# Optimization experiments

Hardware: AMD Instinct MI355X
Metric: run time of the kernel (lower is better)

Reference implementation:

```python
import jax, jax.numpy as jnp
import numpy as np

SIZE_DICT = 512
DIM_DICT = 64
TEMPERATURE = 0.5
EPS = 1e-10


def setup_inputs() -> dict:
    key = jax.random.key(0)
    k1, k2, k3 = jax.random.split(key, 3)
    bs, dz, W, H = 32, 64, 32, 32
    z = jax.random.normal(k1, (bs, dz, W, H), dtype=jnp.float32)
    var_q = jnp.ones((1,), dtype=jnp.float32)
    codebook = jax.random.normal(k2, (SIZE_DICT, DIM_DICT), dtype=jnp.float32)
    gumbel_u = jax.random.uniform(k3, (bs * W * H, SIZE_DICT), dtype=jnp.float32)
    return {"z_from_encoder": z, "var_q": var_q, "codebook": codebook, "gumbel_u": gumbel_u}


def reference(z_from_encoder, var_q, codebook, gumbel_u):
    bs, dz, W, H = z_from_encoder.shape
    # permute to channels-last and flatten: [N, D]
    z_flat = jnp.transpose(z_from_encoder, (0, 2, 3, 1)).reshape(-1, dz)
    # precision with clamping as in torch code
    precision_q = jnp.clip(1.0 / jnp.clip(var_q, 1e-5, None), None, 1e5)  # [1]
    half_prec = 0.5 * precision_q
    # squared euclidean distances to codebook: [N, K]
    dist = (jnp.sum(z_flat ** 2, axis=1, keepdims=True)
            + jnp.sum(codebook ** 2, axis=1)
            - 2.0 * z_flat @ codebook.T)
    logit = -half_prec * dist
    logit = logit - jnp.max(logit, axis=-1, keepdims=True)
    logit = jnp.clip(logit, -50.0, 50.0)
    probabilities = jax.nn.softmax(logit, axis=-1)
    log_probabilities = jax.nn.log_softmax(logit, axis=-1)
    # Gumbel-softmax sampling (training path)
    g = -jnp.log(-jnp.log(gumbel_u + EPS) + EPS)
    encodings = jax.nn.softmax((logit + g) / TEMPERATURE, axis=-1)
    # soft codebook lookup
    z_quantized = (encodings @ codebook).reshape(bs, W, H, dz)
    z_to_decoder = jnp.transpose(z_quantized, (0, 3, 1, 2))  # [bs, D, W, H]
    # discrete KLD term: sum_{n,k} p log p / bs
    kld_discrete = jnp.sum(probabilities * log_probabilities) / bs
    # continuous KLD term: mean over batch of weighted squared error
    kld_continuous = jnp.mean(
        jnp.sum((z_from_encoder - z_to_decoder) ** 2 * half_prec, axis=(1, 2, 3)))
    loss = kld_discrete + kld_continuous
    # perplexity from detached probabilities
    avg_probs = jnp.clip(jnp.mean(jax.lax.stop_gradient(probabilities), axis=0), 1e-10, None)
    perplexity = jnp.exp(-jnp.sum(avg_probs * jnp.log(avg_probs + 1e-10)))
    return z_to_decoder, loss, perplexity
```

## Files before the change

kernel.cpp:

```cpp
#include <hip/hip_runtime.h>


typedef _Float16 half8 __attribute__((ext_vector_type(8)));
typedef float f32x4 __attribute__((ext_vector_type(4)));

#define WS_B1   4096
#define WS_B2   20480
#define WS_PROB 36864
#define WS_LOSS 299008
#define WS_RED  303104
#define WS_NEED 319488

#define ZC_OFF  0
#define ES_OFF  9216
#define ZQ_OFF  50176
#define PR_OFF  83968
#define RM_OFF  86016
#define RS_OFF  87040
#define RP_OFF  88064
#define LB_OFF  89088
#define SMEM_PRE 89152
#define SMEM_FB  155136

#define LOG2E 1.4426950408889634f
#define LN2   0.6931471805599453f
#define C2G   1.4426950408889634e-10f

__device__ __forceinline__ float half_prec(const float* var_q) {
  float vq = var_q[0];
  float pq = fminf(1.0f / fmaxf(vq, 1e-5f), 1e5f);
  return 0.5f * pq;
}

__global__ void k_pre(const float* __restrict__ var_q,
                      const float* __restrict__ cb,
                      float* __restrict__ ws, int pre) {
  int t = threadIdx.x, wg = blockIdx.x;
  if (wg == 0) {
    float hp = half_prec(var_q);
    if (t == 0) ws[512] = 0.0f;
    ws[516 + t] = 0.0f;
    const float4* row = (const float4*)(cb + t * 64);
    float s = 0.0f;
    #pragma unroll
    for (int i = 0; i < 16; ++i) {
      float4 v = row[i];
      s += v.x*v.x + v.y*v.y + v.z*v.z + v.w*v.w;
    }
    ws[t] = hp * s * LOG2E;
  }
  if (!pre) return;
  int gid = wg * 512 + t;
  if (gid < 4096) {
    int l = gid & 63, grp = gid >> 6;
    int tt = grp >> 1, kk = grp & 1;
    int cc = l & 15, gg = l >> 4;
    const float* src = cb + (cc*32 + tt)*64 + kk*32 + gg*8;
    float4 v0 = *(const float4*)src;
    float4 v1 = *(const float4*)(src + 4);
    half8 h = { (_Float16)v0.x, (_Float16)v0.y, (_Float16)v0.z, (_Float16)v0.w,
                (_Float16)v1.x, (_Float16)v1.y, (_Float16)v1.z, (_Float16)v1.w };
    ((half8*)(ws + WS_B1))[gid] = h;
  } else {
    int F = gid - 4096;
    int l = F & 63, grp = F >> 6;
    int kt = grp >> 2, nt = grp & 3;
    int cc = l & 15, gg = l >> 4;
    int dim = nt*16 + cc;
    half8 h;
    #pragma unroll
    for (int j = 0; j < 8; ++j) {
      int kap = gg*8 + j;
      int code = ((kap & 15) << 5) + 2*kt + (kap >> 4);
      h[j] = (_Float16)cb[code*64 + dim];
    }
    ((half8*)(ws + WS_B2))[F] = h;
  }
}

__global__ __launch_bounds__(1024) void k_main_pre(
    const float* __restrict__ z, const float* __restrict__ vq,
    const float* __restrict__ cb, const float* __restrict__ gu,
    float* __restrict__ out, float* __restrict__ ws)
{
  extern __shared__ char smem[];
  float* pr   = (float*)(smem + PR_OFF);
  float* redM = (float*)(smem + RM_OFF);
  float* redS = (float*)(smem + RS_OFF);
  float* redP = (float*)(smem + RP_OFF);
  float* lb   = (float*)(smem + LB_OFF);

  const int tid  = threadIdx.x;
  const int lane = tid & 63;
  const int wv   = tid >> 6;
  const int e    = wv & 3;
  const int p    = wv >> 2;
  const int c    = lane & 15;
  const int g    = lane >> 4;

  if (tid < 512) pr[tid] = 0.0f;

  const half8* B1 = (const half8*)(ws + WS_B1);
  const half8* B2 = (const half8*)(ws + WS_B2);

  const float hp   = half_prec(vq);
  const float s2hp = 2.0f * hp * LOG2E;

  const int row0 = (blockIdx.x * 4 + p) * 16;
  const int b    = row0 >> 10;
  const int wh0  = row0 & 1023;

  _Float16* zc = (_Float16*)(smem + ZC_OFF + p * 2304);

  float zr[4];
  {
    const float* zp = z + ((size_t)(b*64 + lane) << 10) + wh0 + 4*e;
    float4 v0 = *(const float4*)zp;
    zr[0]=v0.x; zr[1]=v0.y; zr[2]=v0.z; zr[3]=v0.w;
  }
  #pragma unroll
  for (int s = 0; s < 4; ++s) zc[(4*e + s)*72 + lane] = (_Float16)(zr[s] * s2hp);

  __syncthreads();

  f32x4 acc[8];
  {
    const float4* hn = (const float4*)(ws + c*32 + 8*e);
    #pragma unroll
    for (int u = 0; u < 2; ++u) {
      float4 h4 = hn[u];
      acc[4*u+0] = (f32x4){-h4.x, -h4.x, -h4.x, -h4.x};
      acc[4*u+1] = (f32x4){-h4.y, -h4.y, -h4.y, -h4.y};
      acc[4*u+2] = (f32x4){-h4.z, -h4.z, -h4.z, -h4.z};
      acc[4*u+3] = (f32x4){-h4.w, -h4.w, -h4.w, -h4.w};
    }
  }

  half8 zA0 = *(const half8*)(zc + c*72 + g*8);
  half8 zA1 = *(const half8*)(zc + c*72 + 32 + g*8);

  #pragma unroll
  for (int t = 0; t < 8; ++t) {
    int tt = 8*e + t;
    acc[t] = __builtin_amdgcn_mfma_f32_16x16x32_f16(zA0, B1[(tt*2+0)*64 + lane], acc[t], 0, 0, 0);
    acc[t] = __builtin_amdgcn_mfma_f32_16x16x32_f16(zA1, B1[(tt*2+1)*64 + lane], acc[t], 0, 0, 0);
  }

  const int rix = p*64 + e*16;

  #pragma unroll
  for (int q = 0; q < 4; ++q) {
    float m = acc[0][q];
    #pragma unroll
    for (int t = 1; t < 8; ++t) m = fmaxf(m, acc[t][q]);
    #pragma unroll
    for (int o = 8; o > 0; o >>= 1) m = fmaxf(m, __shfl_xor(m, o));
    if (c == 0) redM[rix + 4*g + q] = m;
  }
  __syncthreads();
  float mq[4];
  #pragma unroll
  for (int q = 0; q < 4; ++q) {
    int ix = p*64 + 4*g + q;
    mq[q] = fmaxf(fmaxf(redM[ix], redM[ix+16]), fmaxf(redM[ix+32], redM[ix+48]));
  }

  {
    float s1[4] = {0,0,0,0}, pl[4] = {0,0,0,0};
    #pragma unroll
    for (int t = 0; t < 8; ++t)
      #pragma unroll
      for (int q = 0; q < 4; ++q) {
        float l = acc[t][q] - mq[q];
        float ev = exp2f(l);
        s1[q] += ev;
        pl[q] = fmaf(ev, l, pl[q]);
        acc[t][q] = ev;
      }
    #pragma unroll
    for (int q = 0; q < 4; ++q) {
      #pragma unroll
      for (int o = 8; o > 0; o >>= 1) { s1[q] += __shfl_xor(s1[q], o); pl[q] += __shfl_xor(pl[q], o); }
      if (c == 0) { redS[rix + 4*g + q] = s1[q]; redP[rix + 4*g + q] = pl[q]; }
    }
  }
  __syncthreads();
  float kd = 0.0f, inv1[4];
  #pragma unroll
  for (int q = 0; q < 4; ++q) {
    int ix = p*64 + 4*g + q;
    float S = (redS[ix] + redS[ix+16]) + (redS[ix+32] + redS[ix+48]);
    float P = (redP[ix] + redP[ix+16]) + (redP[ix+32] + redP[ix+48]);
    inv1[q] = 1.0f / S;
    kd += P * inv1[q] - __log2f(S);
  }

  #pragma unroll
  for (int t = 0; t < 8; ++t) {
    float v = 0.0f;
    #pragma unroll
    for (int q = 0; q < 4; ++q) v = fmaf(acc[t][q], inv1[q], v);
    v += __shfl_xor(v, 16);
    v += __shfl_xor(v, 32);
    if (g == 0) atomicAdd(&pr[(8*e + t)*16 + c], v);
  }

  #pragma unroll
  for (int q = 0; q < 4; ++q) {
    const float4* ub = (const float4*)(gu + ((size_t)(row0 + 4*g + q))*512 + c*32 + 8*e);
    #pragma unroll
    for (int tt = 0; tt < 2; ++tt) {
      float4 u4 = ub[tt];
      float y0 = C2G - __log2f(u4.x + 1e-10f);
      float y1 = C2G - __log2f(u4.y + 1e-10f);
      float y2 = C2G - __log2f(u4.z + 1e-10f);
      float y3 = C2G - __log2f(u4.w + 1e-10f);
      float t0 = acc[4*tt+0][q] * __builtin_amdgcn_rcpf(y0);
      float t1 = acc[4*tt+1][q] * __builtin_amdgcn_rcpf(y1);
      float t2 = acc[4*tt+2][q] * __builtin_amdgcn_rcpf(y2);
      float t3 = acc[4*tt+3][q] * __builtin_amdgcn_rcpf(y3);
      acc[4*tt+0][q] = t0*t0;
      acc[4*tt+1][q] = t1*t1;
      acc[4*tt+2][q] = t2*t2;
      acc[4*tt+3][q] = t3*t3;
    }
  }

  __syncthreads();

  #pragma unroll
  for (int q = 0; q < 4; ++q) {
    float s = 0.0f;
    #pragma unroll
    for (int t = 0; t < 8; ++t) s += acc[t][q];
    #pragma unroll
    for (int o = 8; o > 0; o >>= 1) s += __shfl_xor(s, o);
    if (c == 0) redS[rix + 4*g + q] = s;
  }
  __syncthreads();
  #pragma unroll
  for (int q = 0; q < 4; ++q) {
    int ix = p*64 + 4*g + q;
    float inv = 1.0f / ((redS[ix] + redS[ix+16]) + (redS[ix+32] + redS[ix+48]));
    #pragma unroll
    for (int t = 0; t < 8; ++t) acc[t][q] *= inv;
  }

  f32x4 zacc[4];
  #pragma unroll
  for (int nt = 0; nt < 4; ++nt) zacc[nt] = (f32x4){0.f, 0.f, 0.f, 0.f};

  _Float16* myES = (_Float16*)(smem + ES_OFF + wv * 2560);
  #pragma unroll
  for (int k = 0; k < 4; ++k) {
    _Float16* eS = myES + (k & 1) * 640;
    #pragma unroll
    for (int tb = 0; tb < 2; ++tb)
      #pragma unroll
      for (int q = 0; q < 4; ++q)
        eS[(4*g + q)*40 + 16*tb + c] = (_Float16)acc[2*k + tb][q];
    half8 ea = *(const half8*)(eS + c*40 + g*8);
    int kt = 4*e + k;
    #pragma unroll
    for (int nt = 0; nt < 4; ++nt)
      zacc[nt] = __builtin_amdgcn_mfma_f32_16x16x32_f16(ea, B2[(kt*4 + nt)*64 + lane], zacc[nt], 0, 0, 0);
  }

  float* zqA = (float*)(smem + ZQ_OFF + p * 8448);
  float* zqB = zqA + 1056;
  if (e & 1) {
    float* zqX = (e == 1) ? zqA : zqB;
    #pragma unroll
    for (int nt = 0; nt < 4; ++nt)
      #pragma unroll
      for (int q = 0; q < 4; ++q)
        zqX[(4*g + q)*66 + nt*16 + c] = zacc[nt][q];
  }
  __syncthreads();
  if (!(e & 1)) {
    float* zqX = (e == 0) ? zqA : zqB;
    #pragma unroll
    for (int nt = 0; nt < 4; ++nt)
      #pragma unroll
      for (int q = 0; q < 4; ++q)
        zqX[(4*g + q)*66 + nt*16 + c] += zacc[nt][q];
  }
  __syncthreads();

  float kc = 0.0f;
  {
    float* orow = out + ((size_t)(b*64 + lane) << 10) + wh0 + 4*e;
    float4 ov;
    ov.x = zqA[(4*e + 0)*66 + lane] + zqB[(4*e + 0)*66 + lane];
    ov.y = zqA[(4*e + 1)*66 + lane] + zqB[(4*e + 1)*66 + lane];
    ov.z = zqA[(4*e + 2)*66 + lane] + zqB[(4*e + 2)*66 + lane];
    ov.w = zqA[(4*e + 3)*66 + lane] + zqB[(4*e + 3)*66 + lane];
    float d;
    d = zr[0]-ov.x; kc = fmaf(d,d,kc);  d = zr[1]-ov.y; kc = fmaf(d,d,kc);
    d = zr[2]-ov.z; kc = fmaf(d,d,kc);  d = zr[3]-ov.w; kc = fmaf(d,d,kc);
    *(float4*)orow = ov;
  }
  kc *= hp;

  float lv = ((e == 0) ? kd * (0.0625f * LN2) : 0.0f) + kc;
  #pragma unroll
  for (int o = 32; o > 0; o >>= 1) lv += __shfl_xor(lv, o);
  if (lane == 0) lb[p*4 + e] = lv;
  __syncthreads();
  if (e == 0 && lane == 0)
    ws[WS_LOSS + blockIdx.x*4 + p] = (lb[p*4+0] + lb[p*4+1]) + (lb[p*4+2] + lb[p*4+3]);

  if (tid < 512) ws[WS_PROB + (size_t)blockIdx.x*512 + tid] = pr[tid];
}

__global__ __launch_bounds__(512) void k_main_fb(
    const float* __restrict__ z, const float* __restrict__ vq,
    const float* __restrict__ cb, const float* __restrict__ gu,
    float* __restrict__ out, float* __restrict__ ws)
{
  extern __shared__ char smem[];
  constexpr int CB = 131072;
  char*  chunkAll = smem + CB;
  float* pr   = (float*)(smem + CB + 20480);
  float* redM = (float*)(smem + CB + 22528);
  float* redS = (float*)(smem + CB + 23040);
  float* redP = (float*)(smem + CB + 23552);

  const int tid  = threadIdx.x;
  const int lane = tid & 63;
  const int wv   = tid >> 6;
  const int h    = wv & 1;
  const int p    = wv >> 1;
  const int c    = lane & 15;
  const int g    = lane >> 4;

  pr[tid] = 0.0f;

  _Float16* lB1 = (_Float16*)smem;
  _Float16* lB2 = (_Float16*)(smem + 65536);
  #pragma unroll
  for (int i = 0; i < 8; ++i) {
    int F = tid + 512*i;
    int l = F & 63, grp = F >> 6;
    int t = grp >> 1, kk = grp & 1;
    int cc = l & 15, gg = l >> 4;
    const float* src = cb + (cc*32 + t)*64 + kk*32 + gg*8;
    float4 v0 = *(const float4*)src;
    float4 v1 = *(const float4*)(src + 4);
    half8 hh = { (_Float16)v0.x, (_Float16)v0.y, (_Float16)v0.z, (_Float16)v0.w,
                 (_Float16)v1.x, (_Float16)v1.y, (_Float16)v1.z, (_Float16)v1.w };
    ((half8*)lB1)[F] = hh;
  }
  #pragma unroll
  for (int i = 0; i < 8; ++i) {
    int F = tid + 512*i;
    int l = F & 63, grp = F >> 6;
    int kt = grp >> 2, nt = grp & 3;
    int cc = l & 15, gg = l >> 4;
    int dim = nt*16 + cc;
    half8 hh;
    #pragma unroll
    for (int j = 0; j < 8; ++j) {
      int kap = gg*8 + j;
      int code = ((kap & 15) << 5) + 2*kt + (kap >> 4);
      hh[j] = (_Float16)cb[code*64 + dim];
    }
    ((half8*)lB2)[F] = hh;
  }
  const half8* B1 = (const half8*)lB1;
  const half8* B2 = (const half8*)lB2;

  const float hp   = half_prec(vq);
  const float s2hp = 2.0f * hp * LOG2E;

  const int row0 = (blockIdx.x * 4 + p) * 16;
  const int b    = row0 >> 10;
  const int wh0  = row0 & 1023;

  _Float16* zc = (_Float16*)(chunkAll + p * 5120);

  float zr[8];
  {
    const float* zp = z + ((size_t)(b*64 + lane) << 10) + wh0 + 8*h;
    float4 v0 = *(const float4*)zp;
    float4 v1 = *(const float4*)(zp + 4);
    zr[0]=v0.x; zr[1]=v0.y; zr[2]=v0.z; zr[3]=v0.w;
    zr[4]=v1.x; zr[5]=v1.y; zr[6]=v1.z; zr[7]=v1.w;
  }
  #pragma unroll
  for (int s = 0; s < 8; ++s) zc[(8*h + s)*72 + lane] = (_Float16)(zr[s] * s2hp);

  __syncthreads();

  f32x4 acc[16];
  {
    const float4* hn = (const float4*)(ws + c*32 + h*16);
    #pragma unroll
    for (int u = 0; u < 4; ++u) {
      float4 h4 = hn[u];
      acc[4*u+0] = (f32x4){-h4.x, -h4.x, -h4.x, -h4.x};
      acc[4*u+1] = (f32x4){-h4.y, -h4.y, -h4.y, -h4.y};
      acc[4*u+2] = (f32x4){-h4.z, -h4.z, -h4.z, -h4.z};
      acc[4*u+3] = (f32x4){-h4.w, -h4.w, -h4.w, -h4.w};
    }
  }

  half8 zA0 = *(const half8*)(zc + c*72 + g*8);
  half8 zA1 = *(const half8*)(zc + c*72 + 32 + g*8);

  #pragma unroll
  for (int t = 0; t < 16; ++t) {
    int tt = h*16 + t;
    acc[t] = __builtin_amdgcn_mfma_f32_16x16x32_f16(zA0, B1[(tt*2+0)*64 + lane], acc[t], 0, 0, 0);
    acc[t] = __builtin_amdgcn_mfma_f32_16x16x32_f16(zA1, B1[(tt*2+1)*64 + lane], acc[t], 0, 0, 0);
  }

  const int rix = p*32 + h*16;

  #pragma unroll
  for (int q = 0; q < 4; ++q) {
    float m = acc[0][q];
    #pragma unroll
    for (int t = 1; t < 16; ++t) m = fmaxf(m, acc[t][q]);
    #pragma unroll
    for (int o = 8; o > 0; o >>= 1) m = fmaxf(m, __shfl_xor(m, o));
    if (c == 0) redM[rix + 4*g + q] = m;
  }
  __syncthreads();
  float mq[4];
  #pragma unroll
  for (int q = 0; q < 4; ++q)
    mq[q] = fmaxf(redM[p*32 + 4*g + q], redM[p*32 + 16 + 4*g + q]);

  {
    float s1[4] = {0,0,0,0}, pl[4] = {0,0,0,0};
    #pragma unroll
    for (int t = 0; t < 16; ++t)
      #pragma unroll
      for (int q = 0; q < 4; ++q) {
        float l = acc[t][q] - mq[q];
        float ev = exp2f(l);
        s1[q] += ev;
        pl[q] = fmaf(ev, l, pl[q]);
        acc[t][q] = ev;
      }
    #pragma unroll
    for (int q = 0; q < 4; ++q) {
      #pragma unroll
      for (int o = 8; o > 0; o >>= 1) { s1[q] += __shfl_xor(s1[q], o); pl[q] += __shfl_xor(pl[q], o); }
      if (c == 0) { redS[rix + 4*g + q] = s1[q]; redP[rix + 4*g + q] = pl[q]; }
    }
  }
  __syncthreads();
  float kd = 0.0f, inv1[4];
  #pragma unroll
  for (int q = 0; q < 4; ++q) {
    float S = redS[p*32 + 4*g + q] + redS[p*32 + 16 + 4*g + q];
    float P = redP[p*32 + 4*g + q] + redP[p*32 + 16 + 4*g + q];
    inv1[q] = 1.0f / S;
    kd += P * inv1[q] - __log2f(S);
  }

  #pragma unroll
  for (int t = 0; t < 16; ++t) {
    float v = 0.0f;
    #pragma unroll
    for (int q = 0; q < 4; ++q) v = fmaf(acc[t][q], inv1[q], v);
    v += __shfl_xor(v, 16);
    v += __shfl_xor(v, 32);
    if (g == 0) atomicAdd(&pr[(h*16 + t)*16 + c], v);
  }

  #pragma unroll
  for (int q = 0; q < 4; ++q) {
    const float4* ub = (const float4*)(gu + ((size_t)(row0 + 4*g + q))*512 + c*32 + h*16);
    #pragma unroll
    for (int tt = 0; tt < 4; ++tt) {
      float4 u4 = ub[tt];
      float y0 = C2G - __log2f(u4.x + 1e-10f);
      float y1 = C2G - __log2f(u4.y + 1e-10f);
      float y2 = C2G - __log2f(u4.z + 1e-10f);
      float y3 = C2G - __log2f(u4.w + 1e-10f);
      float t0 = acc[4*tt+0][q] * __builtin_amdgcn_rcpf(y0);
      float t1 = acc[4*tt+1][q] * __builtin_amdgcn_rcpf(y1);
      float t2 = acc[4*tt+2][q] * __builtin_amdgcn_rcpf(y2);
      float t3 = acc[4*tt+3][q] * __builtin_amdgcn_rcpf(y3);
      acc[4*tt+0][q] = t0*t0;
      acc[4*tt+1][q] = t1*t1;
      acc[4*tt+2][q] = t2*t2;
      acc[4*tt+3][q] = t3*t3;
    }
  }

  __syncthreads();

  #pragma unroll
  for (int q = 0; q < 4; ++q) {
    float s = 0.0f;
    #pragma unroll
    for (int t = 0; t < 16; ++t) s += acc[t][q];
    #pragma unroll
    for (int o = 8; o > 0; o >>= 1) s += __shfl_xor(s, o);
    if (c == 0) redS[rix + 4*g + q] = s;
  }
  __syncthreads();
  #pragma unroll
  for (int q = 0; q < 4; ++q) {
    float inv = 1.0f / (redS[p*32 + 4*g + q] + redS[p*32 + 16 + 4*g + q]);
    #pragma unroll
    for (int t = 0; t < 16; ++t) acc[t][q] *= inv;
  }

  f32x4 zacc[4];
  #pragma unroll
  for (int nt = 0; nt < 4; ++nt) zacc[nt] = (f32x4){0.f, 0.f, 0.f, 0.f};

  _Float16* myES = (_Float16*)(chunkAll + wv * 2560);
  #pragma unroll
  for (int k = 0; k < 8; ++k) {
    _Float16* eS = myES + (k & 1) * 640;
    #pragma unroll
    for (int tb = 0; tb < 2; ++tb)
      #pragma unroll
      for (int q = 0; q < 4; ++q)
        eS[(4*g + q)*40 + 16*tb + c] = (_Float16)acc[2*k + tb][q];
    half8 ea = *(const half8*)(eS + c*40 + g*8);
    int kt = h*8 + k;
    #pragma unroll
    for (int nt = 0; nt < 4; ++nt)
      zacc[nt] = __builtin_amdgcn_mfma_f32_16x16x32_f16(ea, B2[(kt*4 + nt)*64 + lane], zacc[nt], 0, 0, 0);
  }

  __syncthreads();
  float* zqx = (float*)chunkAll + p * 1056;
  if (h) {
    #pragma unroll
    for (int nt = 0; nt < 4; ++nt)
      #pragma unroll
      for (int q = 0; q < 4; ++q)
        zqx[(4*g + q)*66 + nt*16 + c] = zacc[nt][q];
  }
  __syncthreads();
  if (!h) {
    #pragma unroll
    for (int nt = 0; nt < 4; ++nt)
      #pragma unroll
      for (int q = 0; q < 4; ++q)
        zqx[(4*g + q)*66 + nt*16 + c] += zacc[nt][q];
  }
  __syncthreads();

  float kc = 0.0f;
  {
    float* orow = out + ((size_t)(b*64 + lane) << 10) + wh0 + 8*h;
    float4 o0, o1;
    o0.x = zqx[(8*h + 0)*66 + lane]; o0.y = zqx[(8*h + 1)*66 + lane];
    o0.z = zqx[(8*h + 2)*66 + lane]; o0.w = zqx[(8*h + 3)*66 + lane];
    o1.x = zqx[(8*h + 4)*66 + lane]; o1.y = zqx[(8*h + 5)*66 + lane];
    o1.z = zqx[(8*h + 6)*66 + lane]; o1.w = zqx[(8*h + 7)*66 + lane];
    float d;
    d = zr[0]-o0.x; kc = fmaf(d,d,kc);  d = zr[1]-o0.y; kc = fmaf(d,d,kc);
    d = zr[2]-o0.z; kc = fmaf(d,d,kc);  d = zr[3]-o0.w; kc = fmaf(d,d,kc);
    d = zr[4]-o1.x; kc = fmaf(d,d,kc);  d = zr[5]-o1.y; kc = fmaf(d,d,kc);
    d = zr[6]-o1.z; kc = fmaf(d,d,kc);  d = zr[7]-o1.w; kc = fmaf(d,d,kc);
    *(float4*)orow       = o0;
    *(float4*)(orow + 4) = o1;
  }
  kc *= hp;

  float lv = (h ? 0.0f : kd * (0.0625f * LN2)) + kc;
  #pragma unroll
  for (int o = 32; o > 0; o >>= 1) lv += __shfl_xor(lv, o);
  if (lane == 0) atomicAdd(&ws[512], lv);

  __syncthreads();
  atomicAdd(ws + 516 + tid, pr[tid]);
}

__global__ void k_red(float* __restrict__ ws) {
  int gix = blockIdx.x, t = threadIdx.x;
  float s = 0.0f;
  #pragma unroll 4
  for (int i = 0; i < 16; ++i) s += ws[WS_PROB + (size_t)(gix*16 + i)*512 + t];
  ws[WS_RED + gix*512 + t] = s;
}

__global__ void k_fin(const float* __restrict__ ws, float* __restrict__ out, int pre) {
  __shared__ float redH[16], redL[16];
  int t = threadIdx.x;
  float h = 0.0f, l = 0.0f;
  if (pre) {
    if (t < 512) {
      float s = 0.0f;
      #pragma unroll
      for (int g = 0; g < 32; ++g) s += ws[WS_RED + g*512 + t];
      float a = fmaxf(s * (1.0f/32768.0f), 1e-10f);
      h = -a * __logf(a + 1e-10f);
    } else {
      int x = t - 512;
      #pragma unroll
      for (int i = 0; i < 4; ++i) l += ws[WS_LOSS + x + 512*i];
    }
  } else {
    if (t < 512) {
      float a = fmaxf(ws[516 + t] * (1.0f/32768.0f), 1e-10f);
      h = -a * __logf(a + 1e-10f);
    } else if (t == 512) {
      l = ws[512];
    }
  }
  #pragma unroll
  for (int o = 32; o > 0; o >>= 1) { h += __shfl_xor(h, o); l += __shfl_xor(l, o); }
  if ((t & 63) == 0) { redH[t >> 6] = h; redL[t >> 6] = l; }
  __syncthreads();
  if (t == 0) {
    float H = 0.0f, L = 0.0f;
    #pragma unroll
    for (int i = 0; i < 16; ++i) { H += redH[i]; L += redL[i]; }
    out[2097152] = L * (1.0f/32.0f);
    out[2097153] = __expf(H);
  }
}

extern "C" void kernel_launch(void* const* d_in, const int* in_sizes, int n_in,
                              void* d_out, int out_size, void* d_ws, size_t ws_size,
                              hipStream_t stream) {
  const float* z  = (const float*)d_in[0];
  const float* vq = (const float*)d_in[1];
  const float* cb = (const float*)d_in[2];
  const float* gu = (const float*)d_in[3];
  float* out = (float*)d_out;
  float* ws  = (float*)d_ws;
  int pre = (ws_size >= (size_t)WS_NEED * 4) ? 1 : 0;

  hipLaunchKernelGGL(k_pre, dim3(16), dim3(512), 0, stream, vq, cb, ws, pre);
  if (pre) {
    hipFuncSetAttribute((const void*)k_main_pre, hipFuncAttributeMaxDynamicSharedMemorySize, SMEM_PRE);
    hipLaunchKernelGGL(k_main_pre, dim3(512), dim3(1024), SMEM_PRE, stream, z, vq, cb, gu, out, ws);
    hipLaunchKernelGGL(k_red, dim3(32), dim3(512), 0, stream, ws);
  } else {
    hipFuncSetAttribute((const void*)k_main_fb, hipFuncAttributeMaxDynamicSharedMemorySize, SMEM_FB);
    hipLaunchKernelGGL(k_main_fb, dim3(512), dim3(512), SMEM_FB, stream, z, vq, cb, gu, out, ws);
  }
  hipLaunchKernelGGL(k_fin, dim3(1), dim3(1024), 0, stream, ws, out, pre);
}
```

Measured before the change: 62.52 us.

## Stage codebook in LDS via async loads and process two row groups per block

The main kernel now runs 512-thread blocks with 256 workgroups. Each block copies the preprocessed fp16 codebook tiles into LDS with global_load_lds and loops over two 64-row groups, so each codebook copy is reused instead of read from global memory per MFMA. Each wave now covers 16 code tiles instead of 8, which raises register pressure. The gumbel noise loads are double-buffered ahead of use in both the main and fallback kernels. The LDS footprint grows to about 155KB, which limits each CU to one block and reduces occupancy.

```diff
diff --git a/kernel.cpp b/kernel.cpp
--- a/kernel.cpp
+++ b/kernel.cpp
@@ -1,4 +1,5 @@
 #include <hip/hip_runtime.h>
+#include <stdint.h>
 
 
 typedef _Float16 half8 __attribute__((ext_vector_type(8)));
@@ -7,20 +8,16 @@
 #define WS_B1   4096
 #define WS_B2   20480
 #define WS_PROB 36864
-#define WS_LOSS 299008
+#define WS_LOSS 167936
 #define WS_RED  303104
 #define WS_NEED 319488
 
-#define ZC_OFF  0
-#define ES_OFF  9216
-#define ZQ_OFF  50176
-#define PR_OFF  83968
-#define RM_OFF  86016
-#define RS_OFF  87040
-#define RP_OFF  88064
-#define LB_OFF  89088
-#define SMEM_PRE 89152
-#define SMEM_FB  155136
+#define CH_OFF  131072
+#define PR_OFF  151552
+#define RM_OFF  153600
+#define RS_OFF  154112
+#define RP_OFF  154624
+#define SMEM_ALL 155136
 
 #define LOG2E 1.4426950408889634f
 #define LN2   0.6931471805599453f
@@ -30,6 +27,12 @@
   float vq = var_q[0];
   float pq = fminf(1.0f / fmaxf(vq, 1e-5f), 1e5f);
   return 0.5f * pq;
+}
+
+__device__ __forceinline__ void async16(void* l, const void* g) {
+  __builtin_amdgcn_global_load_lds(
+      (const __attribute__((address_space(1))) uint32_t*)g,
+      (__attribute__((address_space(3))) uint32_t*)l, 16, 0, 0);
 }
 
 __global__ void k_pre(const float* __restrict__ var_q,
@@ -78,239 +81,258 @@
   }
 }
 
-__global__ __launch_bounds__(1024) void k_main_pre(
+__global__ __launch_bounds__(512) void k_main_pre(
     const float* __restrict__ z, const float* __restrict__ vq,
     const float* __restrict__ cb, const float* __restrict__ gu,
     float* __restrict__ out, float* __restrict__ ws)
 {
   extern __shared__ char smem[];
+  char*  chunkAll = smem + CH_OFF;
   float* pr   = (float*)(smem + PR_OFF);
   float* redM = (float*)(smem + RM_OFF);
   float* redS = (float*)(smem + RS_OFF);
   float* redP = (float*)(smem + RP_OFF);
-  float* lb   = (float*)(smem + LB_OFF);
 
   const int tid  = threadIdx.x;
   const int lane = tid & 63;
   const int wv   = tid >> 6;
-  const int e    = wv & 3;
-  const int p    = wv >> 2;
+  const int h    = wv & 1;
+  const int p    = wv >> 1;
   const int c    = lane & 15;
   const int g    = lane >> 4;
-
-  if (tid < 512) pr[tid] = 0.0f;
-
-  const half8* B1 = (const half8*)(ws + WS_B1);
-  const half8* B2 = (const half8*)(ws + WS_B2);
+  const int rix  = p*32 + h*16;
+
+  pr[tid] = 0.0f;
+
+  {
+    const char* wsb = (const char*)(ws + WS_B1);
+    #pragma unroll
+    for (int i = 0; i < 16; ++i) {
+      int L = i*512 + tid;
+      async16(smem + (size_t)L*16, wsb + (size_t)L*16);
+    }
+  }
+  const half8* B1 = (const half8*)smem;
+  const half8* B2 = (const half8*)(smem + 65536);
 
   const float hp   = half_prec(vq);
   const float s2hp = 2.0f * hp * LOG2E;
 
-  const int row0 = (blockIdx.x * 4 + p) * 16;
-  const int b    = row0 >> 10;
-  const int wh0  = row0 & 1023;
-
-  _Float16* zc = (_Float16*)(smem + ZC_OFF + p * 2304);
-
-  float zr[4];
-  {
-    const float* zp = z + ((size_t)(b*64 + lane) << 10) + wh0 + 4*e;
-    float4 v0 = *(const float4*)zp;
-    zr[0]=v0.x; zr[1]=v0.y; zr[2]=v0.z; zr[3]=v0.w;
-  }
-  #pragma unroll
-  for (int s = 0; s < 4; ++s) zc[(4*e + s)*72 + lane] = (_Float16)(zr[s] * s2hp);
-
-  __syncthreads();
-
-  f32x4 acc[8];
-  {
-    const float4* hn = (const float4*)(ws + c*32 + 8*e);
-    #pragma unroll
-    for (int u = 0; u < 2; ++u) {
-      float4 h4 = hn[u];
-      acc[4*u+0] = (f32x4){-h4.x, -h4.x, -h4.x, -h4.x};
-      acc[4*u+1] = (f32x4){-h4.y, -h4.y, -h4.y, -h4.y};
-      acc[4*u+2] = (f32x4){-h4.z, -h4.z, -h4.z, -h4.z};
-      acc[4*u+3] = (f32x4){-h4.w, -h4.w, -h4.w, -h4.w};
-    }
-  }
-
-  half8 zA0 = *(const half8*)(zc + c*72 + g*8);
-  half8 zA1 = *(const half8*)(zc + c*72 + 32 + g*8);
-
-  #pragma unroll
-  for (int t = 0; t < 8; ++t) {
-    int tt = 8*e + t;
-    acc[t] = __builtin_amdgcn_mfma_f32_16x16x32_f16(zA0, B1[(tt*2+0)*64 + lane], acc[t], 0, 0, 0);
-    acc[t] = __builtin_amdgcn_mfma_f32_16x16x32_f16(zA1, B1[(tt*2+1)*64 + lane], acc[t], 0, 0, 0);
-  }
-
-  const int rix = p*64 + e*16;
-
-  #pragma unroll
-  for (int q = 0; q < 4; ++q) {
-    float m = acc[0][q];
-    #pragma unroll
-    for (int t = 1; t < 8; ++t) m = fmaxf(m, acc[t][q]);
-    #pragma unroll
-    for (int o = 8; o > 0; o >>= 1) m = fmaxf(m, __shfl_xor(m, o));
-    if (c == 0) redM[rix + 4*g + q] = m;
-  }
-  __syncthreads();
-  float mq[4];
-  #pragma unroll
-  for (int q = 0; q < 4; ++q) {
-    int ix = p*64 + 4*g + q;
-    mq[q] = fmaxf(fmaxf(redM[ix], redM[ix+16]), fmaxf(redM[ix+32], redM[ix+48]));
-  }
-
-  {
-    float s1[4] = {0,0,0,0}, pl[4] = {0,0,0,0};
-    #pragma unroll
-    for (int t = 0; t < 8; ++t)
+  for (int it = 0; it < 2; ++it) {
+    const int row0 = (blockIdx.x*8 + it*4 + p) * 16;
+    const int b    = row0 >> 10;
+    const int wh0  = row0 & 1023;
+
+    _Float16* zc = (_Float16*)(chunkAll + p * 5120);
+
+    float zr[8];
+    {
+      const float* zp = z + ((size_t)(b*64 + lane) << 10) + wh0 + 8*h;
+      float4 v0 = *(const float4*)zp;
+      float4 v1 = *(const float4*)(zp + 4);
+      zr[0]=v0.x; zr[1]=v0.y; zr[2]=v0.z; zr[3]=v0.w;
+      zr[4]=v1.x; zr[5]=v1.y; zr[6]=v1.z; zr[7]=v1.w;
+    }
+    #pragma unroll
+    for (int s = 0; s < 8; ++s) zc[(8*h + s)*72 + lane] = (_Float16)(zr[s] * s2hp);
+
+    __syncthreads();
+
+    f32x4 acc[16];
+    {
+      const float4* hn = (const float4*)(ws + c*32 + h*16);
+      #pragma unroll
+      for (int u = 0; u < 4; ++u) {
+        float4 h4 = hn[u];
+        acc[4*u+0] = (f32x4){-h4.x, -h4.x, -h4.x, -h4.x};
+        acc[4*u+1] = (f32x4){-h4.y, -h4.y, -h4.y, -h4.y};
+        acc[4*u+2] = (f32x4){-h4.z, -h4.z, -h4.z, -h4.z};
+        acc[4*u+3] = (f32x4){-h4.w, -h4.w, -h4.w, -h4.w};
+      }
+    }
+
+    half8 zA0 = *(const half8*)(zc + c*72 + g*8);
+    half8 zA1 = *(const half8*)(zc + c*72 + 32 + g*8);
+
+    #pragma unroll
+    for (int t = 0; t < 16; ++t) {
+      int tt = h*16 + t;
+      acc[t] = __builtin_amdgcn_mfma_f32_16x16x32_f16(zA0, B1[(tt*2+0)*64 + lane], acc[t], 0, 0, 0);
+      acc[t] = __builtin_amdgcn_mfma_f32_16x16x32_f16(zA1, B1[(tt*2+1)*64 + lane], acc[t], 0, 0, 0);
+    }
+
+    const float* gub = gu + ((size_t)(row0 + 4*g))*512 + c*32 + h*16;
+    float4 ubA[4], ubB[4];
+    #pragma unroll
+    for (int tt = 0; tt < 4; ++tt) ubA[tt] = *(const float4*)(gub + tt*4);
+
+    #pragma unroll
+    for (int q = 0; q < 4; ++q) {
+      float m = acc[0][q];
+      #pragma unroll
+      for (int t = 1; t < 16; ++t) m = fmaxf(m, acc[t][q]);
+      #pragma unroll
+      for (int o = 8; o > 0; o >>= 1) m = fmaxf(m, __shfl_xor(m, o));
+      if (c == 0) redM[rix + 4*g + q] = m;
+    }
+    __syncthreads();
+    float mq[4];
+    #pragma unroll
+    for (int q = 0; q < 4; ++q)
+      mq[q] = fmaxf(redM[p*32 + 4*g + q], redM[p*32 + 16 + 4*g + q]);
+
+    {
+      float s1[4] = {0,0,0,0}, pl[4] = {0,0,0,0};
+      #pragma unroll
+      for (int t = 0; t < 16; ++t)
+        #pragma unroll
+        for (int q = 0; q < 4; ++q) {
+          float l = acc[t][q] - mq[q];
+          float e = exp2f(l);
+          s1[q] += e;
+          pl[q] = fmaf(e, l, pl[q]);
+          acc[t][q] = e;
+        }
       #pragma unroll
       for (int q = 0; q < 4; ++q) {
-        float l = acc[t][q] - mq[q];
-        float ev = exp2f(l);
-        s1[q] += ev;
-        pl[q] = fmaf(ev, l, pl[q]);
-        acc[t][q] = ev;
+        #pragma unroll
+        for (int o = 8; o > 0; o >>= 1) { s1[q] += __shfl_xor(s1[q], o); pl[q] += __shfl_xor(pl[q], o); }
+        if (c == 0) { redS[rix + 4*g + q] = s1[q]; redP[rix + 4*g + q] = pl[q]; }
       }
+    }
+    __syncthreads();
+    float kd = 0.0f, inv1[4];
     #pragma unroll
     for (int q = 0; q < 4; ++q) {
-      #pragma unroll
-      for (int o = 8; o > 0; o >>= 1) { s1[q] += __shfl_xor(s1[q], o); pl[q] += __shfl_xor(pl[q], o); }
-      if (c == 0) { redS[rix + 4*g + q] = s1[q]; redP[rix + 4*g + q] = pl[q]; }
-    }
-  }
-  __syncthreads();
-  float kd = 0.0f, inv1[4];
-  #pragma unroll
-  for (int q = 0; q < 4; ++q) {
-    int ix = p*64 + 4*g + q;
-    float S = (redS[ix] + redS[ix+16]) + (redS[ix+32] + redS[ix+48]);
-    float P = (redP[ix] + redP[ix+16]) + (redP[ix+32] + redP[ix+48]);
-    inv1[q] = 1.0f / S;
-    kd += P * inv1[q] - __log2f(S);
-  }
-
-  #pragma unroll
-  for (int t = 0; t < 8; ++t) {
-    float v = 0.0f;
-    #pragma unroll
-    for (int q = 0; q < 4; ++q) v = fmaf(acc[t][q], inv1[q], v);
-    v += __shfl_xor(v, 16);
-    v += __shfl_xor(v, 32);
-    if (g == 0) atomicAdd(&pr[(8*e + t)*16 + c], v);
-  }
-
-  #pragma unroll
-  for (int q = 0; q < 4; ++q) {
-    const float4* ub = (const float4*)(gu + ((size_t)(row0 + 4*g + q))*512 + c*32 + 8*e);
-    #pragma unroll
-    for (int tt = 0; tt < 2; ++tt) {
-      float4 u4 = ub[tt];
-      float y0 = C2G - __log2f(u4.x + 1e-10f);
-      float y1 = C2G - __log2f(u4.y + 1e-10f);
-      float y2 = C2G - __log2f(u4.z + 1e-10f);
-      float y3 = C2G - __log2f(u4.w + 1e-10f);
-      float t0 = acc[4*tt+0][q] * __builtin_amdgcn_rcpf(y0);
-      float t1 = acc[4*tt+1][q] * __builtin_amdgcn_rcpf(y1);
-      float t2 = acc[4*tt+2][q] * __builtin_amdgcn_rcpf(y2);
-      float t3 = acc[4*tt+3][q] * __builtin_amdgcn_rcpf(y3);
-      acc[4*tt+0][q] = t0*t0;
-      acc[4*tt+1][q] = t1*t1;
-      acc[4*tt+2][q] = t2*t2;
-      acc[4*tt+3][q] = t3*t3;
-    }
-  }
-
-  __syncthreads();
-
-  #pragma unroll
-  for (int q = 0; q < 4; ++q) {
-    float s = 0.0f;
-    #pragma unroll
-    for (int t = 0; t < 8; ++t) s += acc[t][q];
-    #pragma unroll
-    for (int o = 8; o > 0; o >>= 1) s += __shfl_xor(s, o);
-    if (c == 0) redS[rix + 4*g + q] = s;
-  }
-  __syncthreads();
-  #pragma unroll
-  for (int q = 0; q < 4; ++q) {
-    int ix = p*64 + 4*g + q;
-    float inv = 1.0f / ((redS[ix] + redS[ix+16]) + (redS[ix+32] + redS[ix+48]));
-    #pragma unroll
-    for (int t = 0; t < 8; ++t) acc[t][q] *= inv;
-  }
-
-  f32x4 zacc[4];
-  #pragma unroll
-  for (int nt = 0; nt < 4; ++nt) zacc[nt] = (f32x4){0.f, 0.f, 0.f, 0.f};
-
-  _Float16* myES = (_Float16*)(smem + ES_OFF + wv * 2560);
-  #pragma unroll
-  for (int k = 0; k < 4; ++k) {
-    _Float16* eS = myES + (k & 1) * 640;
-    #pragma unroll
-    for (int tb = 0; tb < 2; ++tb)
-      #pragma unroll
-      for (int q = 0; q < 4; ++q)
-        eS[(4*g + q)*40 + 16*tb + c] = (_Float16)acc[2*k + tb][q];
-    half8 ea = *(const half8*)(eS + c*40 + g*8);
-    int kt = 4*e + k;
-    #pragma unroll
-    for (int nt = 0; nt < 4; ++nt)
-      zacc[nt] = __builtin_amdgcn_mfma_f32_16x16x32_f16(ea, B2[(kt*4 + nt)*64 + lane], zacc[nt], 0, 0, 0);
-  }
-
-  float* zqA = (float*)(smem + ZQ_OFF + p * 8448);
-  float* zqB = zqA + 1056;
-  if (e & 1) {
-    float* zqX = (e == 1) ? zqA : zqB;
-    #pragma unroll
-    for (int nt = 0; nt < 4; ++nt)
-      #pragma unroll
-      for (int q = 0; q < 4; ++q)
-        zqX[(4*g + q)*66 + nt*16 + c] = zacc[nt][q];
-  }
-  __syncthreads();
-  if (!(e & 1)) {
-    float* zqX = (e == 0) ? zqA : zqB;
-    #pragma unroll
-    for (int nt = 0; nt < 4; ++nt)
-      #pragma unroll
-      for (int q = 0; q < 4; ++q)
-        zqX[(4*g + q)*66 + nt*16 + c] += zacc[nt][q];
-  }
-  __syncthreads();
-
-  float kc = 0.0f;
-  {
-    float* orow = out + ((size_t)(b*64 + lane) << 10) + wh0 + 4*e;
-    float4 ov;
-    ov.x = zqA[(4*e + 0)*66 + lane] + zqB[(4*e + 0)*66 + lane];
-    ov.y = zqA[(4*e + 1)*66 + lane] + zqB[(4*e + 1)*66 + lane];
-    ov.z = zqA[(4*e + 2)*66 + lane] + zqB[(4*e + 2)*66 + lane];
-    ov.w = zqA[(4*e + 3)*66 + lane] + zqB[(4*e + 3)*66 + lane];
-    float d;
-    d = zr[0]-ov.x; kc = fmaf(d,d,kc);  d = zr[1]-ov.y; kc = fmaf(d,d,kc);
-    d = zr[2]-ov.z; kc = fmaf(d,d,kc);  d = zr[3]-ov.w; kc = fmaf(d,d,kc);
-    *(float4*)orow = ov;
-  }
-  kc *= hp;
-
-  float lv = ((e == 0) ? kd * (0.0625f * LN2) : 0.0f) + kc;
-  #pragma unroll
-  for (int o = 32; o > 0; o >>= 1) lv += __shfl_xor(lv, o);
-  if (lane == 0) lb[p*4 + e] = lv;
-  __syncthreads();
-  if (e == 0 && lane == 0)
-    ws[WS_LOSS + blockIdx.x*4 + p] = (lb[p*4+0] + lb[p*4+1]) + (lb[p*4+2] + lb[p*4+3]);
-
-  if (tid < 512) ws[WS_PROB + (size_t)blockIdx.x*512 + tid] = pr[tid];
+      float S = redS[p*32 + 4*g + q] + redS[p*32 + 16 + 4*g + q];
+      float P = redP[p*32 + 4*g + q] + redP[p*32 + 16 + 4*g + q];
+      inv1[q] = 1.0f / S;
+      kd += P * inv1[q] - __log2f(S);
+    }
+
+    #pragma unroll
+    for (int t = 0; t < 16; ++t) {
+      float v = 0.0f;
+      #pragma unroll
+      for (int q = 0; q < 4; ++q) v = fmaf(acc[t][q], inv1[q], v);
+      v += __shfl_xor(v, 16);
+      v += __shfl_xor(v, 32);
+      if (g == 0) atomicAdd(&pr[(h*16 + t)*16 + c], v);
+    }
+
+    #pragma unroll
+    for (int q = 0; q < 4; ++q) {
+      const float4* cur = (q & 1) ? ubB : ubA;
+      float4*       nxt = (q & 1) ? ubA : ubB;
+      if (q < 3) {
+        #pragma unroll
+        for (int tt = 0; tt < 4; ++tt) nxt[tt] = *(const float4*)(gub + (q+1)*512 + tt*4);
+      }
+      #pragma unroll
+      for (int tt = 0; tt < 4; ++tt) {
+        float4 u4 = cur[tt];
+        float y0 = C2G - __log2f(u4.x + 1e-10f);
+        float y1 = C2G - __log2f(u4.y + 1e-10f);
+        float y2 = C2G - __log2f(u4.z + 1e-10f);
+        float y3 = C2G - __log2f(u4.w + 1e-10f);
+        float t0 = acc[4*tt+0][q] * __builtin_amdgcn_rcpf(y0);
+        float t1 = acc[4*tt+1][q] * __builtin_amdgcn_rcpf(y1);
+        float t2 = acc[4*tt+2][q] * __builtin_amdgcn_rcpf(y2);
+        float t3 = acc[4*tt+3][q] * __builtin_amdgcn_rcpf(y3);
+        acc[4*tt+0][q] = t0*t0;
+        acc[4*tt+1][q] = t1*t1;
+        acc[4*tt+2][q] = t2*t2;
+        acc[4*tt+3][q] = t3*t3;
+      }
+    }
+
+    __syncthreads();
+
+    #pragma unroll
+    for (int q = 0; q < 4; ++q) {
+      float s = 0.0f;
+      #pragma unroll
+      for (int t = 0; t < 16; ++t) s += acc[t][q];
+      #pragma unroll
+      for (int o = 8; o > 0; o >>= 1) s += __shfl_xor(s, o);
+      if (c == 0) redS[rix + 4*g + q] = s;
+    }
+    __syncthreads();
+    #pragma unroll
+    for (int q = 0; q < 4; ++q) {
+      float inv = 1.0f / (redS[p*32 + 4*g + q] + redS[p*32 + 16 + 4*g + q]);
+      #pragma unroll
+      for (int t = 0; t < 16; ++t) acc[t][q] *= inv;
+    }
+
+    f32x4 zacc[4];
+    #pragma unroll
+    for (int nt = 0; nt < 4; ++nt) zacc[nt] = (f32x4){0.f, 0.f, 0.f, 0.f};
+
+    _Float16* myES = (_Float16*)(chunkAll + wv * 2560);
+    #pragma unroll
+    for (int k = 0; k < 8; ++k) {
+      _Float16* eS = myES + (k & 1) * 640;
+      #pragma unroll
+      for (int tb = 0; tb < 2; ++tb)
+        #pragma unroll
+        for (int q = 0; q < 4; ++q)
+          eS[(4*g + q)*40 + 16*tb + c] = (_Float16)acc[2*k + tb][q];
+      half8 ea = *(const half8*)(eS + c*40 + g*8);
+      int kt = h*8 + k;
+      #pragma unroll
+      for (int nt = 0; nt < 4; ++nt)
+        zacc[nt] = __builtin_amdgcn_mfma_f32_16x16x32_f16(ea, B2[(kt*4 + nt)*64 + lane], zacc[nt], 0, 0, 0);
+    }
+
+    __syncthreads();
+    float* zqx = (float*)chunkAll + p * 1056;
+    if (h) {
+      #pragma unroll
+      for (int nt = 0; nt < 4; ++nt)
+        #pragma unroll
+        for (int q = 0; q < 4; ++q)
+          zqx[(4*g + q)*66 + nt*16 + c] = zacc[nt][q];
+    }
+    __syncthreads();
+    if (!h) {
+      #pragma unroll
+      for (int nt = 0; nt < 4; ++nt)
+        #pragma unroll
+        for (int q = 0; q < 4; ++q) {
+          int ix = (4*g + q)*66 + nt*16 + c;
+          zqx[ix] += zacc[nt][q];
+        }
+    }
+    __syncthreads();
+
+    float kc = 0.0f;
+    {
+      float* orow = out + ((size_t)(b*64 + lane) << 10) + wh0 + 8*h;
+      float4 o0, o1;
+      o0.x = zqx[(8*h + 0)*66 + lane]; o0.y = zqx[(8*h + 1)*66 + lane];
+      o0.z = zqx[(8*h + 2)*66 + lane]; o0.w = zqx[(8*h + 3)*66 + lane];
+      o1.x = zqx[(8*h + 4)*66 + lane]; o1.y = zqx[(8*h + 5)*66 + lane];
+      o1.z = zqx[(8*h + 6)*66 + lane]; o1.w = zqx[(8*h + 7)*66 + lane];
+      float d;
+      d = zr[0]-o0.x; kc = fmaf(d,d,kc);  d = zr[1]-o0.y; kc = fmaf(d,d,kc);
+      d = zr[2]-o0.z; kc = fmaf(d,d,kc);  d = zr[3]-o0.w; kc = fmaf(d,d,kc);
+      d = zr[4]-o1.x; kc = fmaf(d,d,kc);  d = zr[5]-o1.y; kc = fmaf(d,d,kc);
+      d = zr[6]-o1.z; kc = fmaf(d,d,kc);  d = zr[7]-o1.w; kc = fmaf(d,d,kc);
+      *(float4*)orow       = o0;
+      *(float4*)(orow + 4) = o1;
+    }
+    kc *= hp;
+
+    float lv = (h ? 0.0f : kd * (0.0625f * LN2)) + kc;
+    #pragma unroll
+    for (int o = 32; o > 0; o >>= 1) lv += __shfl_xor(lv, o);
+    if (lane == 0) ws[WS_LOSS + ((size_t)blockIdx.x*2 + it)*8 + wv] = lv;
+
+    __syncthreads();
+  }
+
+  ws[WS_PROB + (size_t)blockIdx.x*512 + tid] = pr[tid];
 }
 
 __global__ __launch_bounds__(512) void k_main_fb(
@@ -319,12 +341,11 @@
     float* __restrict__ out, float* __restrict__ ws)
 {
   extern __shared__ char smem[];
-  constexpr int CB = 131072;
-  char*  chunkAll = smem + CB;
-  float* pr   = (float*)(smem + CB + 20480);
-  float* redM = (float*)(smem + CB + 22528);
-  float* redS = (float*)(smem + CB + 23040);
-  float* redP = (float*)(smem + CB + 23552);
+  char*  chunkAll = smem + CH_OFF;
+  float* pr   = (float*)(smem + PR_OFF);
+  float* redM = (float*)(smem + RM_OFF);
+  float* redS = (float*)(smem + RS_OFF);
+  float* redP = (float*)(smem + RP_OFF);
 
   const int tid  = threadIdx.x;
   const int lane = tid & 63;
@@ -415,6 +436,11 @@
     acc[t] = __builtin_amdgcn_mfma_f32_16x16x32_f16(zA1, B1[(tt*2+1)*64 + lane], acc[t], 0, 0, 0);
   }
 
+  const float* gub = gu + ((size_t)(row0 + 4*g))*512 + c*32 + h*16;
+  float4 ubA[4], ubB[4];
+  #pragma unroll
+  for (int tt = 0; tt < 4; ++tt) ubA[tt] = *(const float4*)(gub + tt*4);
+
   const int rix = p*32 + h*16;
 
   #pragma unroll
@@ -439,10 +465,10 @@
       #pragma unroll
       for (int q = 0; q < 4; ++q) {
         float l = acc[t][q] - mq[q];
-        float ev = exp2f(l);
-        s1[q] += ev;
-        pl[q] = fmaf(ev, l, pl[q]);
-        acc[t][q] = ev;
+        float e = exp2f(l);
+        s1[q] += e;
+        pl[q] = fmaf(e, l, pl[q]);
+        acc[t][q] = e;
       }
     #pragma unroll
     for (int q = 0; q < 4; ++q) {
@@ -473,10 +499,15 @@
 
   #pragma unroll
   for (int q = 0; q < 4; ++q) {
-    const float4* ub = (const float4*)(gu + ((size_t)(row0 + 4*g + q))*512 + c*32 + h*16);
+    const float4* cur = (q & 1) ? ubB : ubA;
+    float4*       nxt = (q & 1) ? ubA : ubB;
+    if (q < 3) {
+      #pragma unroll
+      for (int tt = 0; tt < 4; ++tt) nxt[tt] = *(const float4*)(gub + (q+1)*512 + tt*4);
+    }
     #pragma unroll
     for (int tt = 0; tt < 4; ++tt) {
-      float4 u4 = ub[tt];
+      float4 u4 = cur[tt];
       float y0 = C2G - __log2f(u4.x + 1e-10f);
       float y1 = C2G - __log2f(u4.y + 1e-10f);
       float y2 = C2G - __log2f(u4.z + 1e-10f);
@@ -581,7 +612,7 @@
   int gix = blockIdx.x, t = threadIdx.x;
   float s = 0.0f;
   #pragma unroll 4
-  for (int i = 0; i < 16; ++i) s += ws[WS_PROB + (size_t)(gix*16 + i)*512 + t];
+  for (int i = 0; i < 8; ++i) s += ws[WS_PROB + (size_t)(gix*8 + i)*512 + t];
   ws[WS_RED + gix*512 + t] = s;
 }
 
@@ -599,7 +630,7 @@
     } else {
       int x = t - 512;
       #pragma unroll
-      for (int i = 0; i < 4; ++i) l += ws[WS_LOSS + x + 512*i];
+      for (int i = 0; i < 8; ++i) l += ws[WS_LOSS + x + 512*i];
     }
   } else {
     if (t < 512) {
@@ -635,12 +666,12 @@
 
   hipLaunchKernelGGL(k_pre, dim3(16), dim3(512), 0, stream, vq, cb, ws, pre);
   if (pre) {
-    hipFuncSetAttribute((const void*)k_main_pre, hipFuncAttributeMaxDynamicSharedMemorySize, SMEM_PRE);
-    hipLaunchKernelGGL(k_main_pre, dim3(512), dim3(1024), SMEM_PRE, stream, z, vq, cb, gu, out, ws);
+    hipFuncSetAttribute((const void*)k_main_pre, hipFuncAttributeMaxDynamicSharedMemorySize, SMEM_ALL);
+    hipLaunchKernelGGL(k_main_pre, dim3(256), dim3(512), SMEM_ALL, stream, z, vq, cb, gu, out, ws);
     hipLaunchKernelGGL(k_red, dim3(32), dim3(512), 0, stream, ws);
   } else {
-    hipFuncSetAttribute((const void*)k_main_fb, hipFuncAttributeMaxDynamicSharedMemorySize, SMEM_FB);
-    hipLaunchKernelGGL(k_main_fb, dim3(512), dim3(512), SMEM_FB, stream, z, vq, cb, gu, out, ws);
+    hipFuncSetAttribute((const void*)k_main_fb, hipFuncAttributeMaxDynamicSharedMemorySize, SMEM_ALL);
+    hipLaunchKernelGGL(k_main_fb, dim3(512), dim3(512), SMEM_ALL, stream, z, vq, cb, gu, out, ws);
   }
   hipLaunchKernelGGL(k_fin, dim3(1), dim3(1024), 0, stream, ws, out, pre);
 }
```

Result: faster. 57.52 us (-8.0%).
